# Performance work log

Hardware: AMD Instinct MI355X
Metric: run time of the kernel (lower is better)

The kernel has to match this reference:

```python
import jax, jax.numpy as jnp
import numpy as np

N = 100000      # nodes
E = 1600000     # directed edges
F_IN = 128      # node feature dim
H = 128         # hidden dim
C = 16          # classes


def setup_inputs() -> dict:
    key = jax.random.key(0)
    ks = jax.random.split(key, 8)
    s = 1.0 / np.sqrt(H)
    return {
        "x": jax.random.normal(ks[0], (N, F_IN), dtype=jnp.float32),
        "edge_index": jax.random.randint(ks[1], (2, E), 0, N, dtype=jnp.int32),
        "W1": jax.random.normal(ks[2], (F_IN, H), dtype=jnp.float32) * s,
        "b1": jnp.zeros((H,), jnp.float32),
        "W2": jax.random.normal(ks[3], (H, H), dtype=jnp.float32) * s,
        "b2": jnp.zeros((H,), jnp.float32),
        "W3": jax.random.normal(ks[4], (H, H), dtype=jnp.float32) * s,
        "b3": jnp.zeros((H,), jnp.float32),
        "Wfc": jax.random.normal(ks[5], (H, C), dtype=jnp.float32) * s,
        "bfc": jnp.zeros((C,), jnp.float32),
    }


def _gcn_conv(x, W, b, src, dst, norm):
    # x' = b + scatter_add over edges of norm * (x @ W)[src] into dst
    h = x @ W                                   # [N, H] dense GEMM
    msg = h[src] * norm[:, None]                # [E+N, H] gather + scale
    out = jax.ops.segment_sum(msg, dst, num_segments=N)  # scatter-add
    return out + b


def reference(x, edge_index, W1, b1, W2, b2, W3, b3, Wfc, bfc):
    loops = jnp.arange(N, dtype=edge_index.dtype)
    src = jnp.concatenate([edge_index[0], loops])   # [E+N] with self-loops
    dst = jnp.concatenate([edge_index[1], loops])
    # symmetric normalization deg^{-1/2}[src] * deg^{-1/2}[dst] (PyG default)
    deg = jax.ops.segment_sum(jnp.ones_like(dst, dtype=x.dtype), dst, num_segments=N)
    dinv = jax.lax.rsqrt(deg)                       # deg >= 1 due to self-loops
    norm = dinv[src] * dinv[dst]

    h = jax.nn.elu(_gcn_conv(x, W1, b1, src, dst, norm))   # dropout is identity in eval
    h = jax.nn.elu(_gcn_conv(h, W2, b2, src, dst, norm))
    h = jax.nn.elu(_gcn_conv(h, W3, b3, src, dst, norm))
    logits = h @ Wfc + bfc                                  # [N, C]
    return jax.nn.log_softmax(logits, axis=-1)
```

## Files before the change

kernel.cpp:

```cpp
#include <hip/hip_runtime.h>
#include <math.h>

#define HDIM 128
#define CDIM 16
#define CAP 48
#define ASTR 136
#define NBINS 256
#define TILE 2048

typedef unsigned short u16;
typedef unsigned int u32;
typedef __attribute__((ext_vector_type(8))) short short8;
typedef __attribute__((ext_vector_type(4))) float f32x4;

__device__ inline u16 f2bf(float f) {
  u32 u = __float_as_uint(f);
  u += 0x7fffu + ((u >> 16) & 1u);
  return (u16)(u >> 16);
}
__device__ inline float bf_lo(u32 p) { return __uint_as_float(p << 16); }
__device__ inline float bf_hi(u32 p) { return __uint_as_float(p & 0xffff0000u); }
__device__ inline u32 pack2(float a, float b) {
  return (u32)f2bf(a) | ((u32)f2bf(b) << 16);
}
__device__ inline void add8(float* a, uint4 g) {
  a[0] += bf_lo(g.x); a[1] += bf_hi(g.x);
  a[2] += bf_lo(g.y); a[3] += bf_hi(g.y);
  a[4] += bf_lo(g.z); a[5] += bf_hi(g.z);
  a[6] += bf_lo(g.w); a[7] += bf_hi(g.w);
}


__global__ __launch_bounds__(256) void bin_kernel(const int* __restrict__ ei,
                                                  int* __restrict__ cursor,
                                                  int2* __restrict__ bins,
                                                  int binCap, int E, int npb) {
  __shared__ int2 eds[TILE];
  __shared__ int base[NBINS], rank[NBINS], hist[NBINS];
  int tid = threadIdx.x;
  int t0 = blockIdx.x * TILE;
  int n = min(TILE, E - t0);
  for (int i = tid; i < NBINS; i += 256) { hist[i] = 0; rank[i] = 0; }
  __syncthreads();
  for (int i = tid; i < n; i += 256) {
    int s = ei[t0 + i];
    int d = ei[E + t0 + i];
    eds[i] = make_int2(d, s);
    atomicAdd(&hist[d / npb], 1);
  }
  __syncthreads();
  for (int i = tid; i < NBINS; i += 256) {
    int h = hist[i];
    base[i] = h ? atomicAdd(&cursor[i], h) : 0;
  }
  __syncthreads();
  for (int i = tid; i < n; i += 256) {
    int2 e = eds[i];
    int b = e.x / npb;
    int r = base[b] + atomicAdd(&rank[b], 1);
    if (r < binCap) bins[(size_t)b * binCap + r] = e;
  }
}

__global__ __launch_bounds__(256) void fill2_kernel(const int2* __restrict__ bins,
                                                    const int* __restrict__ cursor,
                                                    int binCap, int* __restrict__ deg,
                                                    int* __restrict__ csr) {
  int b = blockIdx.x;
  int cnt = min(cursor[b], binCap);
  const int2* eb = bins + (size_t)b * binCap;
  for (int i = threadIdx.x; i < cnt; i += 256) {
    int2 e = eb[i];
    int p = atomicAdd(&deg[e.x], 1);
    if (p < CAP) csr[(size_t)e.x * CAP + p] = e.y;
  }
}


__global__ void prep_kernel(const float* __restrict__ W0, const float* __restrict__ W1,
                            const float* __restrict__ W2, u16* __restrict__ Wt,
                            const int* __restrict__ deg, float* __restrict__ dinv, int N) {
  int t = blockIdx.x * 256 + threadIdx.x;
  if (t < 3 * HDIM * HDIM) {
    int which = t >> 14, idx = t & 16383;
    int n = idx >> 7, k = idx & 127;
    const float* W = which == 0 ? W0 : (which == 1 ? W1 : W2);
    Wt[(size_t)which * HDIM * HDIM + n * HDIM + k] = f2bf(W[k * HDIM + n]);
  } else {
    int i = t - 3 * HDIM * HDIM;
    if (i < N) dinv[i] = rsqrtf((float)(deg[i] + 1));
  }
}


template <bool FP32IN>
__global__ __launch_bounds__(256) void gemm_k(const void* __restrict__ Xv,
                                              const u16* __restrict__ Wt,
                                              const float* __restrict__ dinv,
                                              u16* __restrict__ G, int N) {
  __shared__ u16 As[64 * ASTR];
  __shared__ u16 Wsm[128 * ASTR];
  int tid = threadIdx.x;
  int row0 = blockIdx.x * 64;

  {
    int r = tid >> 2, c = tid & 3;
    int rg = row0 + r;
    if (rg >= N) rg = N - 1;
    uint4* dst = (uint4*)(As + r * ASTR + c * 32);
    if (FP32IN) {
      const float4* src = (const float4*)((const float*)Xv + (size_t)rg * HDIM + c * 32);
#pragma unroll
      for (int j = 0; j < 4; ++j) {
        float4 a = src[2 * j], b = src[2 * j + 1];
        uint4 o;
        o.x = pack2(a.x, a.y); o.y = pack2(a.z, a.w);
        o.z = pack2(b.x, b.y); o.w = pack2(b.z, b.w);
        dst[j] = o;
      }
    } else {
      const uint4* src = (const uint4*)((const u16*)Xv + (size_t)rg * HDIM + c * 32);
      dst[0] = src[0]; dst[1] = src[1]; dst[2] = src[2]; dst[3] = src[3];
    }
  }
  {
    int r = tid >> 1, h = tid & 1;
    const uint4* src = (const uint4*)(Wt + r * HDIM + h * 64);
    uint4* dst = (uint4*)(Wsm + r * ASTR + h * 64);
#pragma unroll
    for (int i = 0; i < 8; ++i) dst[i] = src[i];
  }
  __syncthreads();

  int w = tid >> 6;
  int l = tid & 63;
  int m = l & 15, q = l >> 4;

  f32x4 acc[8];
#pragma unroll
  for (int i = 0; i < 8; ++i) acc[i] = (f32x4){0.f, 0.f, 0.f, 0.f};

#pragma unroll
  for (int kc = 0; kc < 4; ++kc) {
    short8 af = *(const short8*)(As + (w * 16 + m) * ASTR + kc * 32 + q * 8);
#pragma unroll
    for (int nt = 0; nt < 8; ++nt) {
      short8 bfr = *(const short8*)(Wsm + (nt * 16 + m) * ASTR + kc * 32 + q * 8);
      acc[nt] = __builtin_amdgcn_mfma_f32_16x16x32_bf16(af, bfr, acc[nt], 0, 0, 0);
    }
  }
  __syncthreads();

  float dv[4];
#pragma unroll
  for (int r = 0; r < 4; ++r) {
    int rg = row0 + w * 16 + q * 4 + r;
    dv[r] = dinv[rg < N ? rg : N - 1];
  }
#pragma unroll
  for (int nt = 0; nt < 8; ++nt)
#pragma unroll
    for (int r = 0; r < 4; ++r)
      As[(w * 16 + q * 4 + r) * ASTR + nt * 16 + m] = f2bf(acc[nt][r] * dv[r]);
  __syncthreads();

  {
    int r = tid >> 2, c = tid & 3;
    int rg = row0 + r;
    if (rg < N) {
      uint4* dst = (uint4*)(G + (size_t)rg * HDIM + c * 32);
      const uint4* src = (const uint4*)(As + r * ASTR + c * 32);
      dst[0] = src[0]; dst[1] = src[1]; dst[2] = src[2]; dst[3] = src[3];
    }
  }
}


__device__ inline void gather_node(const u16* __restrict__ G, const int* __restrict__ deg,
                                   const int* __restrict__ csr, const float* __restrict__ dinv,
                                   const float4* __restrict__ b4, int node, int l, float* v) {
  float a[8];
  {
    uint4 s = *(const uint4*)(G + (size_t)node * HDIM + l * 8);
    a[0] = bf_lo(s.x); a[1] = bf_hi(s.x);
    a[2] = bf_lo(s.y); a[3] = bf_hi(s.y);
    a[4] = bf_lo(s.z); a[5] = bf_hi(s.z);
    a[6] = bf_lo(s.w); a[7] = bf_hi(s.w);
  }
  int d = min(deg[node], CAP);
  const int* row = csr + (size_t)node * CAP;
  int i = 0;
  for (; i + 4 <= d; i += 4) {
    int u0 = row[i], u1 = row[i + 1], u2 = row[i + 2], u3 = row[i + 3];
    uint4 g0 = *(const uint4*)(G + (size_t)u0 * HDIM + l * 8);
    uint4 g1 = *(const uint4*)(G + (size_t)u1 * HDIM + l * 8);
    uint4 g2 = *(const uint4*)(G + (size_t)u2 * HDIM + l * 8);
    uint4 g3 = *(const uint4*)(G + (size_t)u3 * HDIM + l * 8);
    add8(a, g0); add8(a, g1); add8(a, g2); add8(a, g3);
  }
  for (; i < d; ++i) {
    uint4 g = *(const uint4*)(G + (size_t)row[i] * HDIM + l * 8);
    add8(a, g);
  }
  float dvn = dinv[node];
  float4 b0 = b4[l * 2], b1 = b4[l * 2 + 1];
  v[0] = fmaf(dvn, a[0], b0.x); v[1] = fmaf(dvn, a[1], b0.y);
  v[2] = fmaf(dvn, a[2], b0.z); v[3] = fmaf(dvn, a[3], b0.w);
  v[4] = fmaf(dvn, a[4], b1.x); v[5] = fmaf(dvn, a[5], b1.y);
  v[6] = fmaf(dvn, a[6], b1.z); v[7] = fmaf(dvn, a[7], b1.w);
#pragma unroll
  for (int j = 0; j < 8; ++j) v[j] = v[j] > 0.f ? v[j] : expm1f(v[j]);
}


__global__ __launch_bounds__(256) void agg_bf(const u16* __restrict__ G,
                                              const int* __restrict__ deg,
                                              const int* __restrict__ csr,
                                              const float* __restrict__ dinv,
                                              const float* __restrict__ b,
                                              u16* __restrict__ out, int N) {
  int node = blockIdx.x * 16 + (threadIdx.x >> 4);
  if (node >= N) return;
  int l = threadIdx.x & 15;
  float v[8];
  gather_node(G, deg, csr, dinv, (const float4*)b, node, l, v);
  uint4 o;
  o.x = pack2(v[0], v[1]); o.y = pack2(v[2], v[3]);
  o.z = pack2(v[4], v[5]); o.w = pack2(v[6], v[7]);
  *(uint4*)(out + (size_t)node * HDIM + l * 8) = o;
}


__global__ __launch_bounds__(256) void agg_fc(const u16* __restrict__ G,
                                              const int* __restrict__ deg,
                                              const int* __restrict__ csr,
                                              const float* __restrict__ dinv,
                                              const float* __restrict__ b,
                                              const float* __restrict__ Wfc,
                                              const float* __restrict__ bfc,
                                              float* __restrict__ out, int N) {
  __shared__ u16 As[16 * ASTR];
  __shared__ float Wl[HDIM * CDIM];
  int tid = threadIdx.x;
  for (int i = tid; i < HDIM * CDIM; i += 256) Wl[i] = Wfc[i];

  int node0 = blockIdx.x * 16;
  int lr = tid >> 4, l = tid & 15;
  int node = node0 + lr;
  if (node < N) {
    float v[8];
    gather_node(G, deg, csr, dinv, (const float4*)b, node, l, v);
    uint4 o;
    o.x = pack2(v[0], v[1]); o.y = pack2(v[2], v[3]);
    o.z = pack2(v[4], v[5]); o.w = pack2(v[6], v[7]);
    *(uint4*)(As + lr * ASTR + l * 8) = o;
  }
  __syncthreads();

  int rg = node0 + lr;
  if (rg >= N) return;
  int c = l;
  const u16* hrow = As + lr * ASTR;
  float acc = bfc[c];
#pragma unroll 4
  for (int k8 = 0; k8 < 16; ++k8) {
    uint4 g = *(const uint4*)(hrow + k8 * 8);
    const float* wk = Wl + (k8 * 8) * CDIM + c;
    acc = fmaf(bf_lo(g.x), wk[0 * CDIM], acc);
    acc = fmaf(bf_hi(g.x), wk[1 * CDIM], acc);
    acc = fmaf(bf_lo(g.y), wk[2 * CDIM], acc);
    acc = fmaf(bf_hi(g.y), wk[3 * CDIM], acc);
    acc = fmaf(bf_lo(g.z), wk[4 * CDIM], acc);
    acc = fmaf(bf_hi(g.z), wk[5 * CDIM], acc);
    acc = fmaf(bf_lo(g.w), wk[6 * CDIM], acc);
    acc = fmaf(bf_hi(g.w), wk[7 * CDIM], acc);
  }
  float mx = acc;
  for (int off = 8; off >= 1; off >>= 1) mx = fmaxf(mx, __shfl_xor(mx, off, 16));
  float ex = expf(acc - mx);
  float ssum = ex;
  for (int off = 8; off >= 1; off >>= 1) ssum += __shfl_xor(ssum, off, 16);
  out[(size_t)rg * CDIM + c] = (acc - mx) - logf(ssum);
}


extern "C" void kernel_launch(void* const* d_in, const int* in_sizes, int n_in,
                              void* d_out, int out_size, void* d_ws, size_t ws_size,
                              hipStream_t stream) {
  const float* x   = (const float*)d_in[0];
  const int*   ei  = (const int*)d_in[1];
  const float* W1  = (const float*)d_in[2];
  const float* b1  = (const float*)d_in[3];
  const float* W2  = (const float*)d_in[4];
  const float* b2  = (const float*)d_in[5];
  const float* W3  = (const float*)d_in[6];
  const float* b3  = (const float*)d_in[7];
  const float* Wfc = (const float*)d_in[8];
  const float* bfc = (const float*)d_in[9];

  const int N = in_sizes[0] / HDIM;
  const int E = in_sizes[1] / 2;
  const int npb = (N + NBINS - 1) / NBINS;
  const int binCap = (E + NBINS - 1) / NBINS + 1024;

  char* ws = (char*)d_ws;
  size_t off = 0;
  auto alloc = [&](size_t bytes) -> void* {
    void* p = ws + off;
    off += (bytes + 511) & ~(size_t)511;
    return p;
  };
  size_t degBytes = ((size_t)N * 4 + 511) & ~(size_t)511;
  int*   deg    = (int*)alloc((size_t)N * 4);
  int*   cursor = (int*)alloc((size_t)NBINS * 4);
  float* dinv   = (float*)alloc((size_t)N * 4);
  int*   csr    = (int*)alloc((size_t)N * CAP * 4);
  int2*  bins   = (int2*)alloc((size_t)NBINS * binCap * 8);
  u16*   Wt     = (u16*)alloc((size_t)3 * HDIM * HDIM * 2);
  u16*   A      = (u16*)alloc((size_t)N * HDIM * 2);
  u16*   B      = (u16*)alloc((size_t)N * HDIM * 2);

  hipMemsetAsync(deg, 0, degBytes + 1024, stream);
  bin_kernel<<<(E + TILE - 1) / TILE, 256, 0, stream>>>(ei, cursor, bins, binCap, E, npb);
  fill2_kernel<<<NBINS, 256, 0, stream>>>(bins, cursor, binCap, deg, csr);
  prep_kernel<<<(3 * HDIM * HDIM + N + 255) / 256, 256, 0, stream>>>(W1, W2, W3, Wt, deg, dinv,
                                                                     N);

  int grid64 = (N + 63) / 64;
  int grid16 = (N + 15) / 16;
  gemm_k<true><<<grid64, 256, 0, stream>>>(x, Wt, dinv, A, N);
  agg_bf<<<grid16, 256, 0, stream>>>(A, deg, csr, dinv, b1, B, N);
  gemm_k<false><<<grid64, 256, 0, stream>>>(B, Wt + HDIM * HDIM, dinv, A, N);
  agg_bf<<<grid16, 256, 0, stream>>>(A, deg, csr, dinv, b2, B, N);
  gemm_k<false><<<grid64, 256, 0, stream>>>(B, Wt + 2 * HDIM * HDIM, dinv, A, N);
  agg_fc<<<grid16, 256, 0, stream>>>(A, deg, csr, dinv, b3, Wfc, bfc, (float*)d_out, N);
}
```

Baseline: 421.7 us.

## Stripe node features into column blocks so aggregation gathers hit L2

Intermediate node features are stored in a striped layout of 8 column blocks of 16 bf16 (32 B per node per stripe) instead of row-major 256 B rows. The aggregation kernel is split per stripe, so each block gathers neighbors from a 3.2 MB stripe that can stay cache resident rather than from the full 25 MB feature array. The final layer's aggregation and FC are split into two kernels, which adds a round trip through global memory. The binning tile size is also doubled.

```diff
diff --git a/kernel.cpp b/kernel.cpp
--- a/kernel.cpp
+++ b/kernel.cpp
@@ -6,7 +6,8 @@
 #define CAP 48
 #define ASTR 136
 #define NBINS 256
-#define TILE 2048
+#define TILE 4096
+#define NSTRIPE 8
 
 typedef unsigned short u16;
 typedef unsigned int u32;
@@ -103,24 +104,31 @@
   int tid = threadIdx.x;
   int row0 = blockIdx.x * 64;
 
-  {
+  if (FP32IN) {
     int r = tid >> 2, c = tid & 3;
     int rg = row0 + r;
     if (rg >= N) rg = N - 1;
     uint4* dst = (uint4*)(As + r * ASTR + c * 32);
-    if (FP32IN) {
-      const float4* src = (const float4*)((const float*)Xv + (size_t)rg * HDIM + c * 32);
-#pragma unroll
-      for (int j = 0; j < 4; ++j) {
-        float4 a = src[2 * j], b = src[2 * j + 1];
-        uint4 o;
-        o.x = pack2(a.x, a.y); o.y = pack2(a.z, a.w);
-        o.z = pack2(b.x, b.y); o.w = pack2(b.z, b.w);
-        dst[j] = o;
-      }
-    } else {
-      const uint4* src = (const uint4*)((const u16*)Xv + (size_t)rg * HDIM + c * 32);
-      dst[0] = src[0]; dst[1] = src[1]; dst[2] = src[2]; dst[3] = src[3];
+    const float4* src = (const float4*)((const float*)Xv + (size_t)rg * HDIM + c * 32);
+#pragma unroll
+    for (int j = 0; j < 4; ++j) {
+      float4 a = src[2 * j], b = src[2 * j + 1];
+      uint4 o;
+      o.x = pack2(a.x, a.y); o.y = pack2(a.z, a.w);
+      o.z = pack2(b.x, b.y); o.w = pack2(b.z, b.w);
+      dst[j] = o;
+    }
+  } else {
+    const u16* Xs = (const u16*)Xv;
+#pragma unroll
+    for (int it = 0; it < 2; ++it) {
+      int p = tid + 256 * it;
+      int s = p >> 6, r = p & 63;
+      int rg = row0 + r;
+      if (rg >= N) rg = N - 1;
+      const uint4* src = (const uint4*)(Xs + ((size_t)s * N + rg) * 16);
+      uint4* dst = (uint4*)(As + r * ASTR + s * 16);
+      dst[0] = src[0]; dst[1] = src[1];
     }
   }
   {
@@ -165,101 +173,99 @@
   __syncthreads();
 
   {
-    int r = tid >> 2, c = tid & 3;
-    int rg = row0 + r;
-    if (rg < N) {
-      uint4* dst = (uint4*)(G + (size_t)rg * HDIM + c * 32);
-      const uint4* src = (const uint4*)(As + r * ASTR + c * 32);
-      dst[0] = src[0]; dst[1] = src[1]; dst[2] = src[2]; dst[3] = src[3];
+#pragma unroll
+    for (int it = 0; it < 2; ++it) {
+      int p = tid + 256 * it;
+      int s = p >> 6, r = p & 63;
+      int rg = row0 + r;
+      if (rg < N) {
+        uint4* dst = (uint4*)(G + ((size_t)s * N + rg) * 16);
+        const uint4* src = (const uint4*)(As + r * ASTR + s * 16);
+        dst[0] = src[0]; dst[1] = src[1];
+      }
     }
   }
 }
 
 
-__device__ inline void gather_node(const u16* __restrict__ G, const int* __restrict__ deg,
-                                   const int* __restrict__ csr, const float* __restrict__ dinv,
-                                   const float4* __restrict__ b4, int node, int l, float* v) {
+__global__ __launch_bounds__(256) void agg_s(const u16* __restrict__ G,
+                                             const int* __restrict__ deg,
+                                             const int* __restrict__ csr,
+                                             const float* __restrict__ dinv,
+                                             const float* __restrict__ bvec,
+                                             u16* __restrict__ Hout, int N) {
+  int stripe = blockIdx.x & 7;
+  int chunk = blockIdx.x >> 3;
+  int lr = threadIdx.x >> 1, h = threadIdx.x & 1;
+  int node = chunk * 128 + lr;
+  if (node >= N) return;
+  const u16* Gst = G + (size_t)stripe * N * 16;
+
   float a[8];
   {
-    uint4 s = *(const uint4*)(G + (size_t)node * HDIM + l * 8);
-    a[0] = bf_lo(s.x); a[1] = bf_hi(s.x);
-    a[2] = bf_lo(s.y); a[3] = bf_hi(s.y);
-    a[4] = bf_lo(s.z); a[5] = bf_hi(s.z);
-    a[6] = bf_lo(s.w); a[7] = bf_hi(s.w);
+    uint4 s0 = *(const uint4*)(Gst + (u32)node * 16 + h * 8);
+    a[0] = bf_lo(s0.x); a[1] = bf_hi(s0.x);
+    a[2] = bf_lo(s0.y); a[3] = bf_hi(s0.y);
+    a[4] = bf_lo(s0.z); a[5] = bf_hi(s0.z);
+    a[6] = bf_lo(s0.w); a[7] = bf_hi(s0.w);
   }
   int d = min(deg[node], CAP);
   const int* row = csr + (size_t)node * CAP;
   int i = 0;
   for (; i + 4 <= d; i += 4) {
-    int u0 = row[i], u1 = row[i + 1], u2 = row[i + 2], u3 = row[i + 3];
-    uint4 g0 = *(const uint4*)(G + (size_t)u0 * HDIM + l * 8);
-    uint4 g1 = *(const uint4*)(G + (size_t)u1 * HDIM + l * 8);
-    uint4 g2 = *(const uint4*)(G + (size_t)u2 * HDIM + l * 8);
-    uint4 g3 = *(const uint4*)(G + (size_t)u3 * HDIM + l * 8);
+    u32 o0 = (u32)row[i + 0] * 16 + h * 8;
+    u32 o1 = (u32)row[i + 1] * 16 + h * 8;
+    u32 o2 = (u32)row[i + 2] * 16 + h * 8;
+    u32 o3 = (u32)row[i + 3] * 16 + h * 8;
+    uint4 g0 = *(const uint4*)(Gst + o0);
+    uint4 g1 = *(const uint4*)(Gst + o1);
+    uint4 g2 = *(const uint4*)(Gst + o2);
+    uint4 g3 = *(const uint4*)(Gst + o3);
     add8(a, g0); add8(a, g1); add8(a, g2); add8(a, g3);
   }
   for (; i < d; ++i) {
-    uint4 g = *(const uint4*)(G + (size_t)row[i] * HDIM + l * 8);
+    uint4 g = *(const uint4*)(Gst + (u32)row[i] * 16 + h * 8);
     add8(a, g);
   }
   float dvn = dinv[node];
-  float4 b0 = b4[l * 2], b1 = b4[l * 2 + 1];
+  const float4* b4 = (const float4*)bvec;
+  float4 b0 = b4[stripe * 4 + h * 2], b1 = b4[stripe * 4 + h * 2 + 1];
+  float v[8];
   v[0] = fmaf(dvn, a[0], b0.x); v[1] = fmaf(dvn, a[1], b0.y);
   v[2] = fmaf(dvn, a[2], b0.z); v[3] = fmaf(dvn, a[3], b0.w);
   v[4] = fmaf(dvn, a[4], b1.x); v[5] = fmaf(dvn, a[5], b1.y);
   v[6] = fmaf(dvn, a[6], b1.z); v[7] = fmaf(dvn, a[7], b1.w);
 #pragma unroll
   for (int j = 0; j < 8; ++j) v[j] = v[j] > 0.f ? v[j] : expm1f(v[j]);
-}
-
-
-__global__ __launch_bounds__(256) void agg_bf(const u16* __restrict__ G,
-                                              const int* __restrict__ deg,
-                                              const int* __restrict__ csr,
-                                              const float* __restrict__ dinv,
-                                              const float* __restrict__ b,
-                                              u16* __restrict__ out, int N) {
-  int node = blockIdx.x * 16 + (threadIdx.x >> 4);
-  if (node >= N) return;
-  int l = threadIdx.x & 15;
-  float v[8];
-  gather_node(G, deg, csr, dinv, (const float4*)b, node, l, v);
   uint4 o;
   o.x = pack2(v[0], v[1]); o.y = pack2(v[2], v[3]);
   o.z = pack2(v[4], v[5]); o.w = pack2(v[6], v[7]);
-  *(uint4*)(out + (size_t)node * HDIM + l * 8) = o;
-}
-
-
-__global__ __launch_bounds__(256) void agg_fc(const u16* __restrict__ G,
-                                              const int* __restrict__ deg,
-                                              const int* __restrict__ csr,
-                                              const float* __restrict__ dinv,
-                                              const float* __restrict__ b,
-                                              const float* __restrict__ Wfc,
-                                              const float* __restrict__ bfc,
-                                              float* __restrict__ out, int N) {
+  *(uint4*)(Hout + (size_t)stripe * N * 16 + (u32)node * 16 + h * 8) = o;
+}
+
+
+__global__ __launch_bounds__(256) void fc_kernel(const u16* __restrict__ Hs,
+                                                 const float* __restrict__ Wfc,
+                                                 const float* __restrict__ bfc,
+                                                 float* __restrict__ out, int N) {
   __shared__ u16 As[16 * ASTR];
   __shared__ float Wl[HDIM * CDIM];
   int tid = threadIdx.x;
   for (int i = tid; i < HDIM * CDIM; i += 256) Wl[i] = Wfc[i];
-
   int node0 = blockIdx.x * 16;
-  int lr = tid >> 4, l = tid & 15;
-  int node = node0 + lr;
-  if (node < N) {
-    float v[8];
-    gather_node(G, deg, csr, dinv, (const float4*)b, node, l, v);
-    uint4 o;
-    o.x = pack2(v[0], v[1]); o.y = pack2(v[2], v[3]);
-    o.z = pack2(v[4], v[5]); o.w = pack2(v[6], v[7]);
-    *(uint4*)(As + lr * ASTR + l * 8) = o;
-  }
-  __syncthreads();
-
+  {
+    int lr = tid >> 4, k = tid & 15;
+    int s = k >> 1, hh = k & 1;
+    int node = node0 + lr;
+    if (node >= N) node = N - 1;
+    const uint4* src = (const uint4*)(Hs + ((size_t)s * N + node) * 16 + hh * 8);
+    *(uint4*)(As + lr * ASTR + k * 8) = src[0];
+  }
+  __syncthreads();
+
+  int lr = tid >> 4, c = tid & 15;
   int rg = node0 + lr;
   if (rg >= N) return;
-  int c = l;
   const u16* hrow = As + lr * ASTR;
   float acc = bfc[c];
 #pragma unroll 4
@@ -327,11 +333,13 @@
                                                                      N);
 
   int grid64 = (N + 63) / 64;
+  int gridAgg = 8 * ((N + 127) / 128);
   int grid16 = (N + 15) / 16;
   gemm_k<true><<<grid64, 256, 0, stream>>>(x, Wt, dinv, A, N);
-  agg_bf<<<grid16, 256, 0, stream>>>(A, deg, csr, dinv, b1, B, N);
+  agg_s<<<gridAgg, 256, 0, stream>>>(A, deg, csr, dinv, b1, B, N);
   gemm_k<false><<<grid64, 256, 0, stream>>>(B, Wt + HDIM * HDIM, dinv, A, N);
-  agg_bf<<<grid16, 256, 0, stream>>>(A, deg, csr, dinv, b2, B, N);
+  agg_s<<<gridAgg, 256, 0, stream>>>(A, deg, csr, dinv, b2, B, N);
   gemm_k<false><<<grid64, 256, 0, stream>>>(B, Wt + 2 * HDIM * HDIM, dinv, A, N);
-  agg_fc<<<grid16, 256, 0, stream>>>(A, deg, csr, dinv, b3, Wfc, bfc, (float*)d_out, N);
-}
+  agg_s<<<gridAgg, 256, 0, stream>>>(A, deg, csr, dinv, b3, B, N);
+  fc_kernel<<<grid16, 256, 0, stream>>>(B, Wfc, bfc, (float*)d_out, N);
+}
```

Result: slower. 566.3 us (+34.3%).
